# Performance work log

Measured on AMD Instinct MI355X. Metric: run time of the kernel, lower is better.

Reference implementation:

```python
import jax, jax.numpy as jnp
import numpy as np
from jax import lax

RATE = 2
KSIZE = 3
FUSE_K = 3
SOFTMAX_SCALE = 10.0
EPS = 1e-8


def extract_patches(x, k, s):
    """ZeroPad2d(1) then unfold: x [B,C,H,W] -> patches [B, oh*ow, C, k, k]."""
    xp = jnp.pad(x, ((0, 0), (0, 0), (1, 1), (1, 1)))
    B, C, Hp, Wp = xp.shape
    oh = (Hp - k) // s + 1
    ow = (Wp - k) // s + 1
    ii = (jnp.arange(oh) * s)[:, None] + jnp.arange(k)[None, :]   # [oh,k]
    jj = (jnp.arange(ow) * s)[:, None] + jnp.arange(k)[None, :]   # [ow,k]
    p = xp[:, :, ii[:, :, None, None], jj[None, None, :, :]]      # [B,C,oh,k,ow,k]
    p = p.transpose(0, 2, 4, 1, 3, 5).reshape(B, oh * ow, C, k, k)
    return p


def _fuse_conv(a, eye):
    # a: [B,1,N,M]; 3x3 identity-diagonal smoothing conv, padding 1
    return lax.conv_general_dilated(a, eye, (1, 1), [(1, 1), (1, 1)],
                                    dimension_numbers=('NCHW', 'OIHW', 'NCHW'))


def contextual_attention(in_data, mask):
    B, C, H, W = in_data.shape
    Cf = C // 2
    f_full = in_data[:, :Cf]          # narrow(1,0,C//2)
    b_full = in_data[:, :Cf]          # source narrows the SAME slice for b
    mask_f = mask.astype(in_data.dtype)
    rate = RATE
    kernel = 2 * rate

    # raw 4x4 patches of full-res background (deconv filters), [B,L,Cf,4,4]
    raw_w = extract_patches(b_full, kernel, rate)

    # nearest downsample by 1/rate == strided slicing
    f = f_full[:, :, ::rate, ::rate]
    b = b_full[:, :, ::rate, ::rate]
    h, w = f.shape[2], f.shape[3]
    L = h * w

    # 3x3 matching patches of downsampled background, L2-normalized per patch
    wpat = extract_patches(b, KSIZE, 1)                              # [B,L,Cf,3,3]
    norm = jnp.sqrt(jnp.sum(wpat * wpat, axis=(2, 3, 4), keepdims=True))
    wn = wpat / jnp.maximum(norm, EPS)

    # per-sample conv2d(xi, wi_normed, padding=1) == patch/patch correlation
    fp = extract_patches(f, KSIZE, 1)                                # [B,hw,Cf,3,3]
    yi = jnp.einsum('bpckl,bqckl->bqp', fp, wn).reshape(B, L, h, w)  # [B,L,h,w]

    # fuse: two diagonal 3x3 smoothing passes over the [L, h*w] score matrix
    eye = jnp.eye(FUSE_K, dtype=in_data.dtype).reshape(1, 1, FUSE_K, FUSE_K)
    A = yi.reshape(B, 1, L, h * w)
    A = _fuse_conv(A, eye)
    A = A.reshape(B, h, w, h, w).transpose(0, 2, 1, 4, 3).reshape(B, 1, w * h, w * h)
    A = _fuse_conv(A, eye)
    A = A.reshape(B, w, h, w, h).transpose(0, 2, 1, 4, 3)
    yi = A.reshape(B, L, h, w)

    # mask gate: mm = 1 where the 3x3 mask patch is all-zero
    mpat = extract_patches(mask_f, KSIZE, 1)[0]                      # [L,1,3,3]
    m_mean = jnp.mean(mpat, axis=(1, 2, 3))                          # [L]
    mm = (m_mean == 0.0).astype(in_data.dtype)[None, :, None, None]
    yi = yi * mm
    yi = jax.nn.softmax(yi * SOFTMAX_SCALE, axis=1)
    yi = yi * mm

    # conv_transpose2d(yi, raw_wi, stride=rate, padding=1) / 4 per sample
    def agg(y1, rw):
        rhs = jnp.flip(rw, (-2, -1)).transpose(1, 0, 2, 3)           # [Cf,L,4,4]
        return lax.conv_general_dilated(y1[None], rhs, (1, 1), [(2, 2), (2, 2)],
                                        lhs_dilation=(rate, rate),
                                        dimension_numbers=('NCHW', 'OIHW', 'NCHW'))[0]
    y = jax.vmap(agg)(yi, raw_w) / 4.0                               # [B,Cf,H,W]

    # masked_fill_(inv_mask, 0) == multiply by {0,1} mask, upsampled to H x W
    mask_up = jnp.repeat(jnp.repeat(mask_f, rate, axis=2), rate, axis=3)
    y = y * mask_up

    return jnp.concatenate([b_full, f_full, y], axis=1)             # [B,3*Cf,H,W]


def setup_inputs() -> dict:
    key = jax.random.key(0)
    k1, k2 = jax.random.split(key)
    in_data = jax.random.normal(k1, (2, 128, 128, 128), dtype=jnp.float32)
    mask = jax.random.randint(k2, (1, 1, 64, 64), 0, 2, dtype=jnp.int32)
    return {"in_data": in_data, "mask": mask}


def reference(in_data, mask):
    return contextual_attention(in_data, mask)
```

## Files before the change

### kernel.cpp

```cpp
#include <hip/hip_runtime.h>
#include <math.h>

#define MAX_SLOTS 64
#define L 4096

#define OFF_CNT   0
#define OFF_LIST  64
#define OFF_FSUB  512
#define OFF_K5    2230784
#define OFF_SF    3869184
#define OFF_W     5966336

__global__ __launch_bounds__(256) void k_fsub(const float* __restrict__ in,
                                              const int* __restrict__ mask,
                                              int* __restrict__ cnt,
                                              int* __restrict__ list,
                                              float* __restrict__ fsub,
                                              float* __restrict__ sf) {
    int idx = blockIdx.x * 256 + threadIdx.x;
    int j = idx & 63;
    int i = (idx >> 6) & 63;
    int c = (idx >> 12) & 63;
    int b = idx >> 18;
    float v = in[(((b * 128 + c) * 128) + 2 * i) * 128 + 2 * j];
    fsub[(size_t)b * 278784 + c * 4356 + (i + 1) * 66 + (j + 1)] = v;
    sf[idx] = 0.f;
    if (idx < 33280) {
        int plane = idx / 260;
        int r = idx - plane * 260;
        int pb = plane >> 6, pc = plane & 63;
        int row, col;
        if (r < 66) { row = 0; col = r; }
        else if (r < 132) { row = 65; col = r - 66; }
        else { int rr = r - 132; row = (rr >> 1) + 1; col = (rr & 1) ? 65 : 0; }
        fsub[(size_t)pb * 278784 + pc * 4356 + row * 66 + col] = 0.f;
    }
    if (blockIdx.x == 0) {
        __shared__ int lcnt;
        if (threadIdx.x == 0) lcnt = 0;
        __syncthreads();
        for (int q = threadIdx.x; q < L; q += 256) {
            int qi = q >> 6, qj = q & 63;
            bool allz = true;
            for (int dy = -1; dy <= 1; ++dy)
                for (int dx = -1; dx <= 1; ++dx) {
                    int y = qi + dy, x = qj + dx;
                    if (y >= 0 && y < 64 && x >= 0 && x < 64)
                        allz = allz && (mask[y * 64 + x] == 0);
                }
            if (allz) {
                int p = atomicAdd(&lcnt, 1);
                if (p < MAX_SLOTS) list[p] = q;
            }
        }
        __syncthreads();
        if (threadIdx.x == 0) *cnt = (lcnt < MAX_SLOTS) ? lcnt : MAX_SLOTS;
    }
}

__global__ __launch_bounds__(256) void k_prep(const float* __restrict__ fsub,
                                              const int* __restrict__ cnt,
                                              const int* __restrict__ list,
                                              float* __restrict__ K5) {
    int slot = blockIdx.x, b = blockIdx.y;
    int tid = threadIdx.x;
    int nact = min(*cnt, MAX_SLOTS);
    if (slot >= nact) {
        for (int t = tid; t < 1600; t += 256) {
            int c = t / 25, e = t - c * 25;
            K5[(((size_t)b * 64 + c) * 64 + slot) * 25 + e] = 0.f;
        }
        return;
    }
    __shared__ float patch9[9 * 576];
    __shared__ int flag9[9];
    if (tid < 9) flag9[tid] = 0;
    __syncthreads();
    int Q = list[slot];
    const float* F = fsub + (size_t)b * 278784;
    int w = tid >> 6, lane = tid & 63;
    for (int combo = w; combo < 9; combo += 4) {
        int d2 = combo / 3 - 1, d1 = combo % 3 - 1;
        int XQ = ((Q & 63) << 6) + (Q >> 6) + d2;
        if (XQ < 0 || XQ >= L) continue;
        int YQ = ((XQ & 63) << 6) + (XQ >> 6);
        int R = YQ + d1;
        if (R < 0 || R >= L) continue;
        if (lane == 0) flag9[combo] = 1;
        int ri = R >> 6, rj = R & 63;
        const float* Fp = F + ri * 66 + rj;
        float vals[9]; float ss = 0.f;
        #pragma unroll
        for (int k = 0; k < 9; ++k) {
            int t = lane + (k << 6);
            int c = t / 9; int tap = t - c * 9;
            int dy = tap / 3, dx = tap - dy * 3;
            float v = Fp[c * 4356 + dy * 66 + dx];
            vals[k] = v; ss += v * v;
        }
        for (int o = 32; o > 0; o >>= 1) ss += __shfl_xor(ss, o);
        float inv = 1.f / fmaxf(sqrtf(ss), 1e-8f);
        float* dst = patch9 + combo * 576;
        #pragma unroll
        for (int k = 0; k < 9; ++k) dst[lane + (k << 6)] = vals[k] * inv;
    }
    __syncthreads();
    for (int t = tid; t < 1600; t += 256) {
        int c = t / 25, e = t - c * 25;
        int oy = e / 5 - 2, ox = e - (e / 5) * 5 - 2;
        float s = 0.f;
        for (int dy = -1; dy <= 1; ++dy) {
            int dd2 = oy - dy; if (dd2 < -1 || dd2 > 1) continue;
            for (int dx = -1; dx <= 1; ++dx) {
                int dd1 = ox - dx; if (dd1 < -1 || dd1 > 1) continue;
                int combo = (dd2 + 1) * 3 + (dd1 + 1);
                if (flag9[combo])
                    s += patch9[combo * 576 + c * 9 + (dy + 1) * 3 + (dx + 1)];
            }
        }
        K5[(((size_t)b * 64 + c) * 64 + slot) * 25 + e] = s;
    }
}

__global__ __launch_bounds__(64) void k_conv(const float* __restrict__ fsub,
                                             const int* __restrict__ cnt,
                                             const float* __restrict__ K5,
                                             float* __restrict__ sf) {
    int r  = blockIdx.x + 1;
    int cg = blockIdx.y;
    int b  = blockIdx.z;
    int j  = threadIdx.x;
    int nact = min(*cnt, MAX_SLOTS);
    if (nact == 0) return;
    int jc = min(max(j, 1), 62);
    const float* F = fsub + (size_t)b * 278784;
    int base = (r - 1) * 66 + (jc - 1);
    bool active = (j >= 1 && j <= 62);
    int P = (r << 6) + j;
    for (int s0 = 0; s0 < nact; s0 += 16) {
        float acc[16];
        #pragma unroll
        for (int s = 0; s < 16; ++s) acc[s] = 0.f;
        #pragma unroll
        for (int cc = 0; cc < 4; ++cc) {
            int c = cg * 4 + cc;
            const float* Fc = F + c * 4356 + base;
            float win[25];
            #pragma unroll
            for (int dy = 0; dy < 5; ++dy)
                #pragma unroll
                for (int dx = 0; dx < 5; ++dx)
                    win[dy * 5 + dx] = Fc[dy * 66 + dx];
            const float* kc = K5 + (((size_t)b * 64 + c) * 64 + s0) * 25;
            #pragma unroll
            for (int s = 0; s < 16; ++s) {
                #pragma unroll
                for (int k = 0; k < 25; ++k)
                    acc[s] += kc[s * 25 + k] * win[k];
            }
        }
        if (active) {
            int smax = min(16, nact - s0);
            for (int s = 0; s < smax; ++s)
                atomicAdd(&sf[((size_t)b * 64 + (s0 + s)) * 4096 + P], acc[s]);
        }
    }
}

__global__ __launch_bounds__(256) void k_border(const float* __restrict__ fsub,
                                                const int* __restrict__ cnt,
                                                const int* __restrict__ list,
                                                float* __restrict__ sf) {
    int combo = blockIdx.x, slot = blockIdx.y, b = blockIdx.z;
    int tid = threadIdx.x;
    int nact = min(*cnt, MAX_SLOTS);
    if (slot >= nact) return;
    int d2 = combo / 3 - 1, d1 = combo % 3 - 1;
    int Q = list[slot];
    int XQ = ((Q & 63) << 6) + (Q >> 6) + d2;
    if (XQ < 0 || XQ >= L) return;
    int YQ = ((XQ & 63) << 6) + (XQ >> 6);
    int R = YQ + d1;
    if (R < 0 || R >= L) return;
    int ri = R >> 6, rj = R & 63;
    const float* F = fsub + (size_t)b * 278784;
    __shared__ float patch[576];
    __shared__ float red[256];
    __shared__ float s_inv;
    const float* Fp = F + ri * 66 + rj;
    auto ld = [&](int t) -> float {
        int c = t / 9; int tap = t - c * 9;
        int dy = tap / 3, dx = tap - dy * 3;
        return Fp[c * 4356 + dy * 66 + dx];
    };
    float v0 = ld(tid), v1 = ld(tid + 256), v2 = (tid < 64) ? ld(tid + 512) : 0.f;
    red[tid] = v0 * v0 + v1 * v1 + v2 * v2;
    __syncthreads();
    if (tid < 64) {
        float a = red[tid] + red[tid + 64] + red[tid + 128] + red[tid + 192];
        for (int o = 32; o > 0; o >>= 1) a += __shfl_xor(a, o);
        if (tid == 0) s_inv = 1.f / fmaxf(sqrtf(a), 1e-8f);
    }
    __syncthreads();
    float inv = s_inv;
    patch[tid] = v0 * inv; patch[tid + 256] = v1 * inv;
    if (tid < 64) patch[tid + 512] = v2 * inv;
    __syncthreads();
    if (tid >= 252) return;
    int i, j;
    if (tid < 64)       { i = 0;  j = tid; }
    else if (tid < 128) { i = 63; j = tid - 64; }
    else if (tid < 190) { i = tid - 127; j = 0; }
    else                { i = tid - 189; j = 63; }
    int P = (i << 6) + j;
    int XP = (j << 6) + i + d2;
    if (XP < 0 || XP >= L) return;
    int YP = ((XP & 63) << 6) + (XP >> 6);
    int Z = YP + d1;
    if (Z < 0 || Z >= L) return;
    int pi = Z >> 6, pj = Z & 63;
    const float* Fz = F + pi * 66 + pj;
    float dot = 0.f;
    #pragma unroll 4
    for (int c = 0; c < 64; ++c) {
        const float* Fc = Fz + c * 4356;
        const float* pc = patch + c * 9;
        dot += Fc[0] * pc[0]   + Fc[1] * pc[1]   + Fc[2] * pc[2];
        dot += Fc[66] * pc[3]  + Fc[67] * pc[4]  + Fc[68] * pc[5];
        dot += Fc[132] * pc[6] + Fc[133] * pc[7] + Fc[134] * pc[8];
    }
    atomicAdd(&sf[((size_t)b * 64 + slot) * 4096 + P], dot);
}

__global__ __launch_bounds__(256) void k_soft(const int* __restrict__ cnt,
                                              const float* __restrict__ sf,
                                              float* __restrict__ wbuf) {
    int idx = blockIdx.x * 256 + threadIdx.x;
    int b = idx >> 12; int P = idx & 4095;
    int nact = min(*cnt, MAX_SLOTS);
    float M = 0.f;
    for (int s = 0; s < nact; ++s) {
        float l = 10.f * sf[((size_t)b * 64 + s) * 4096 + P];
        M = fmaxf(M, l);
    }
    float denom = (float)(L - nact) * expf(-M);
    for (int s = 0; s < nact; ++s) {
        float e = expf(10.f * sf[((size_t)b * 64 + s) * 4096 + P] - M);
        wbuf[((size_t)b * 64 + s) * 4096 + P] = e;
        denom += e;
    }
    float inv = 1.f / denom;
    for (int s = 0; s < nact; ++s)
        wbuf[((size_t)b * 64 + s) * 4096 + P] *= inv;
}

__global__ __launch_bounds__(128) void k_out(const float* __restrict__ in,
                                             const int* __restrict__ mask,
                                             const int* __restrict__ cnt,
                                             const int* __restrict__ list,
                                             const float* __restrict__ wbuf,
                                             float* __restrict__ out) {
    __shared__ float pat8[MAX_SLOTS * 128];
    int u = blockIdx.x, cg = blockIdx.y, b = blockIdx.z;
    int c0 = cg * 8;
    int tid = threadIdx.x;
    int nact = min(*cnt, MAX_SLOTS);
    const float* inb0 = in + (size_t)b * 2097152 + (size_t)c0 * 16384;
    for (int t = tid; t < nact * 128; t += 128) {
        int s = t >> 7; int r = t & 127;
        int cc = r >> 4; int e = r & 15; int aa = e >> 2; int bb = e & 3;
        int q = list[s]; int qi = q >> 6, qj = q & 63;
        int row = 2 * qi - 1 + aa, col = 2 * qj - 1 + bb;
        float v = (row >= 0 && row < 128 && col >= 0 && col < 128)
                  ? inb0[(size_t)cc * 16384 + row * 128 + col] : 0.f;
        pat8[t] = v;
    }
    __syncthreads();
    int v = tid;
    float y[8];
    #pragma unroll
    for (int cc = 0; cc < 8; ++cc) y[cc] = 0.f;
    if (mask[(u >> 1) * 64 + (v >> 1)] != 0 && nact > 0) {
        int pa = (u + 1) & 1, pb = (v + 1) & 1;
        int i0 = (u + 1 - pa) >> 1, j0 = (v + 1 - pb) >> 1;
        for (int s = 0; s < nact; ++s) {
            const float* wrow = wbuf + ((size_t)b * 64 + s) * 4096;
            const float* ps = pat8 + s * 128;
            #pragma unroll
            for (int di = 0; di < 2; ++di) {
                int i = i0 - di; if (i < 0 || i >= 64) continue;
                int aa = pa + 2 * di;
                #pragma unroll
                for (int dj = 0; dj < 2; ++dj) {
                    int j = j0 - dj; if (j < 0 || j >= 64) continue;
                    float wv = wrow[(i << 6) + j];
                    int tap = aa * 4 + pb + 2 * dj;
                    #pragma unroll
                    for (int cc = 0; cc < 8; ++cc)
                        y[cc] += wv * ps[cc * 16 + tap];
                }
            }
        }
        #pragma unroll
        for (int cc = 0; cc < 8; ++cc) y[cc] *= 0.25f;
    }
    size_t ob = (size_t)(b * 192) * 16384 + (size_t)u * 128 + v;
    #pragma unroll
    for (int cc = 0; cc < 8; ++cc) {
        int c = c0 + cc;
        float val = in[(size_t)(b * 128 + c) * 16384 + u * 128 + v];
        out[ob + (size_t)c * 16384] = val;
        out[ob + (size_t)(c + 64) * 16384] = val;
        out[ob + (size_t)(c + 128) * 16384] = y[cc];
    }
}

extern "C" void kernel_launch(void* const* d_in, const int* in_sizes, int n_in,
                              void* d_out, int out_size, void* d_ws, size_t ws_size,
                              hipStream_t stream) {
    const float* in = (const float*)d_in[0];
    const int* mask = (const int*)d_in[1];
    float* out = (float*)d_out;
    char* ws = (char*)d_ws;
    int* cnt    = (int*)(ws + OFF_CNT);
    int* list   = (int*)(ws + OFF_LIST);
    float* fsub = (float*)(ws + OFF_FSUB);
    float* K5   = (float*)(ws + OFF_K5);
    float* sf   = (float*)(ws + OFF_SF);
    float* wbuf = (float*)(ws + OFF_W);

    k_fsub<<<2048, 256, 0, stream>>>(in, mask, cnt, list, fsub, sf);
    k_prep<<<dim3(MAX_SLOTS, 2), 256, 0, stream>>>(fsub, cnt, list, K5);
    k_conv<<<dim3(62, 16, 2), 64, 0, stream>>>(fsub, cnt, K5, sf);
    k_border<<<dim3(9, MAX_SLOTS, 2), 256, 0, stream>>>(fsub, cnt, list, sf);
    k_soft<<<32, 256, 0, stream>>>(cnt, sf, wbuf);
    k_out<<<dim3(128, 8, 2), 128, 0, stream>>>(in, mask, cnt, list, wbuf, out);
}
```

Baseline: 174.6 us.

## Fuse prep, conv, border, softmax and output into one persistent kernel

Merges the five kernels after initialisation into one persistent kernel with 256 blocks, separated by software grid barriers built on atomic counters. K5 preparation and the border scores now run concurrently on separate block ranges. The softmax is folded into the output stage and recomputed on the fly from the scores, so the weight buffer is no longer written and re-read. This removes launch gaps and a round trip through global memory, but it depends on all 256 blocks being resident at once and recomputes expf three times per element.

```diff
diff --git a/kernel.cpp b/kernel.cpp
--- a/kernel.cpp
+++ b/kernel.cpp
@@ -3,18 +3,20 @@
 
 #define MAX_SLOTS 64
 #define L 4096
+#define NB2 256
 
 #define OFF_CNT   0
 #define OFF_LIST  64
+#define OFF_BAR   384
 #define OFF_FSUB  512
 #define OFF_K5    2230784
 #define OFF_SF    3869184
-#define OFF_W     5966336
-
-__global__ __launch_bounds__(256) void k_fsub(const float* __restrict__ in,
+
+__global__ __launch_bounds__(256) void k_init(const float* __restrict__ in,
                                               const int* __restrict__ mask,
                                               int* __restrict__ cnt,
                                               int* __restrict__ list,
+                                              int* __restrict__ bar,
                                               float* __restrict__ fsub,
                                               float* __restrict__ sf) {
     int idx = blockIdx.x * 256 + threadIdx.x;
@@ -36,6 +38,7 @@
         fsub[(size_t)pb * 278784 + pc * 4356 + row * 66 + col] = 0.f;
     }
     if (blockIdx.x == 0) {
+        if (threadIdx.x < 4) bar[threadIdx.x] = 0;
         __shared__ int lcnt;
         if (threadIdx.x == 0) lcnt = 0;
         __syncthreads();
@@ -58,260 +61,285 @@
     }
 }
 
-__global__ __launch_bounds__(256) void k_prep(const float* __restrict__ fsub,
-                                              const int* __restrict__ cnt,
-                                              const int* __restrict__ list,
-                                              float* __restrict__ K5) {
-    int slot = blockIdx.x, b = blockIdx.y;
+__device__ __forceinline__ void grid_barrier(int* bar, int phase) {
+    __syncthreads();
+    __threadfence();
+    if (threadIdx.x == 0) {
+        __hip_atomic_fetch_add(&bar[phase], 1, __ATOMIC_ACQ_REL, __HIP_MEMORY_SCOPE_AGENT);
+        while (__hip_atomic_load(&bar[phase], __ATOMIC_ACQUIRE, __HIP_MEMORY_SCOPE_AGENT) < NB2)
+            __builtin_amdgcn_s_sleep(2);
+    }
+    __syncthreads();
+    __threadfence();
+}
+
+__global__ __launch_bounds__(256, 2) void k_fused(const float* __restrict__ in,
+                                                  const int* __restrict__ mask,
+                                                  const int* __restrict__ cnt,
+                                                  const int* __restrict__ list,
+                                                  int* __restrict__ bar,
+                                                  const float* __restrict__ fsub,
+                                                  float* __restrict__ K5,
+                                                  float* __restrict__ sf,
+                                                  float* __restrict__ out) {
+    __shared__ float smem[8192];
+    __shared__ int iflags[16];
     int tid = threadIdx.x;
+    int blk = blockIdx.x;
     int nact = min(*cnt, MAX_SLOTS);
-    if (slot >= nact) {
-        for (int t = tid; t < 1600; t += 256) {
-            int c = t / 25, e = t - c * 25;
-            K5[(((size_t)b * 64 + c) * 64 + slot) * 25 + e] = 0.f;
-        }
-        return;
-    }
-    __shared__ float patch9[9 * 576];
-    __shared__ int flag9[9];
-    if (tid < 9) flag9[tid] = 0;
-    __syncthreads();
-    int Q = list[slot];
-    const float* F = fsub + (size_t)b * 278784;
-    int w = tid >> 6, lane = tid & 63;
-    for (int combo = w; combo < 9; combo += 4) {
-        int d2 = combo / 3 - 1, d1 = combo % 3 - 1;
-        int XQ = ((Q & 63) << 6) + (Q >> 6) + d2;
-        if (XQ < 0 || XQ >= L) continue;
-        int YQ = ((XQ & 63) << 6) + (XQ >> 6);
-        int R = YQ + d1;
-        if (R < 0 || R >= L) continue;
-        if (lane == 0) flag9[combo] = 1;
-        int ri = R >> 6, rj = R & 63;
-        const float* Fp = F + ri * 66 + rj;
-        float vals[9]; float ss = 0.f;
+
+    if (blk < 128) {
+        int slot = blk & 63, b = blk >> 6;
+        if (slot >= nact) {
+            for (int t = tid; t < 1600; t += 256) {
+                int c = t / 25, e = t - c * 25;
+                K5[(((size_t)b * 64 + c) * 64 + slot) * 25 + e] = 0.f;
+            }
+        } else {
+            float* patch9 = smem;
+            if (tid < 9) iflags[tid] = 0;
+            __syncthreads();
+            int Q = list[slot];
+            const float* F = fsub + (size_t)b * 278784;
+            int w = tid >> 6, lane = tid & 63;
+            for (int combo = w; combo < 9; combo += 4) {
+                int d2 = combo / 3 - 1, d1 = combo % 3 - 1;
+                int XQ = ((Q & 63) << 6) + (Q >> 6) + d2;
+                if (XQ < 0 || XQ >= L) continue;
+                int YQ = ((XQ & 63) << 6) + (XQ >> 6);
+                int R = YQ + d1;
+                if (R < 0 || R >= L) continue;
+                if (lane == 0) iflags[combo] = 1;
+                int ri = R >> 6, rj = R & 63;
+                const float* Fp = F + ri * 66 + rj;
+                float vals[9]; float ss = 0.f;
+                #pragma unroll
+                for (int k = 0; k < 9; ++k) {
+                    int t = lane + (k << 6);
+                    int c = t / 9; int tap = t - c * 9;
+                    int dy = tap / 3, dx = tap - dy * 3;
+                    float v = Fp[c * 4356 + dy * 66 + dx];
+                    vals[k] = v; ss += v * v;
+                }
+                for (int o = 32; o > 0; o >>= 1) ss += __shfl_xor(ss, o);
+                float inv = 1.f / fmaxf(sqrtf(ss), 1e-8f);
+                float* dst = patch9 + combo * 576;
+                #pragma unroll
+                for (int k = 0; k < 9; ++k) dst[lane + (k << 6)] = vals[k] * inv;
+            }
+            __syncthreads();
+            for (int t = tid; t < 1600; t += 256) {
+                int c = t / 25, e = t - c * 25;
+                int oy = e / 5 - 2, ox = e - (e / 5) * 5 - 2;
+                float s = 0.f;
+                for (int dy = -1; dy <= 1; ++dy) {
+                    int dd2 = oy - dy; if (dd2 < -1 || dd2 > 1) continue;
+                    for (int dx = -1; dx <= 1; ++dx) {
+                        int dd1 = ox - dx; if (dd1 < -1 || dd1 > 1) continue;
+                        int combo = (dd2 + 1) * 3 + (dd1 + 1);
+                        if (iflags[combo])
+                            s += patch9[combo * 576 + c * 9 + (dy + 1) * 3 + (dx + 1)];
+                    }
+                }
+                K5[(((size_t)b * 64 + c) * 64 + slot) * 25 + e] = s;
+            }
+        }
+    } else {
+        for (int bt = blk - 128; bt < 1152; bt += 128) {
+            int combo = bt % 9; int rest = bt / 9;
+            int slot = rest & 63, b = rest >> 6;
+            int d2 = combo / 3 - 1, d1 = combo % 3 - 1;
+            int ri = 0, rj = 0;
+            bool valid = (slot < nact);
+            if (valid) {
+                int Q = list[slot];
+                int XQ = ((Q & 63) << 6) + (Q >> 6) + d2;
+                valid = (XQ >= 0 && XQ < L);
+                if (valid) {
+                    int YQ = ((XQ & 63) << 6) + (XQ >> 6);
+                    int R = YQ + d1;
+                    valid = (R >= 0 && R < L);
+                    if (valid) { ri = R >> 6; rj = R & 63; }
+                }
+            }
+            if (!valid) continue;
+            float* patch = smem;
+            float* red = smem + 576;
+            const float* F = fsub + (size_t)b * 278784;
+            const float* Fp = F + ri * 66 + rj;
+            __syncthreads();
+            auto ld = [&](int t) -> float {
+                int c = t / 9; int tap = t - c * 9;
+                int dy = tap / 3, dx = tap - dy * 3;
+                return Fp[c * 4356 + dy * 66 + dx];
+            };
+            float v0 = ld(tid), v1 = ld(tid + 256), v2 = (tid < 64) ? ld(tid + 512) : 0.f;
+            red[tid] = v0 * v0 + v1 * v1 + v2 * v2;
+            __syncthreads();
+            if (tid < 64) {
+                float a = red[tid] + red[tid + 64] + red[tid + 128] + red[tid + 192];
+                for (int o = 32; o > 0; o >>= 1) a += __shfl_xor(a, o);
+                if (tid == 0) smem[832] = 1.f / fmaxf(sqrtf(a), 1e-8f);
+            }
+            __syncthreads();
+            float inv = smem[832];
+            patch[tid] = v0 * inv; patch[tid + 256] = v1 * inv;
+            if (tid < 64) patch[tid + 512] = v2 * inv;
+            __syncthreads();
+            if (tid < 252) {
+                int i, j;
+                if (tid < 64)       { i = 0;  j = tid; }
+                else if (tid < 128) { i = 63; j = tid - 64; }
+                else if (tid < 190) { i = tid - 127; j = 0; }
+                else                { i = tid - 189; j = 63; }
+                int P = (i << 6) + j;
+                int XP = (j << 6) + i + d2;
+                if (XP >= 0 && XP < L) {
+                    int YP = ((XP & 63) << 6) + (XP >> 6);
+                    int Z = YP + d1;
+                    if (Z >= 0 && Z < L) {
+                        int pi = Z >> 6, pj = Z & 63;
+                        const float* Fz = F + pi * 66 + pj;
+                        float dot = 0.f;
+                        #pragma unroll 4
+                        for (int c = 0; c < 64; ++c) {
+                            const float* Fc = Fz + c * 4356;
+                            const float* pc = patch + c * 9;
+                            dot += Fc[0] * pc[0]   + Fc[1] * pc[1]   + Fc[2] * pc[2];
+                            dot += Fc[66] * pc[3]  + Fc[67] * pc[4]  + Fc[68] * pc[5];
+                            dot += Fc[132] * pc[6] + Fc[133] * pc[7] + Fc[134] * pc[8];
+                        }
+                        atomicAdd(&sf[((size_t)b * 64 + slot) * 4096 + P], dot);
+                    }
+                }
+            }
+        }
+    }
+    grid_barrier(bar, 0);
+
+    {
+        int wid = blk * 4 + (tid >> 6);
+        int j = tid & 63;
+        for (int gw = wid; gw < 1984; gw += NB2 * 4) {
+            int r   = 1 + (gw % 62);
+            int cg2 = (gw / 62) & 15;
+            int b   = gw / 992;
+            int jc = min(max(j, 1), 62);
+            const float* F = fsub + (size_t)b * 278784;
+            int base = (r - 1) * 66 + (jc - 1);
+            bool active = (j >= 1 && j <= 62);
+            int P = (r << 6) + j;
+            for (int s0 = 0; s0 < nact; s0 += 16) {
+                float acc[16];
+                #pragma unroll
+                for (int s = 0; s < 16; ++s) acc[s] = 0.f;
+                #pragma unroll
+                for (int cc = 0; cc < 4; ++cc) {
+                    int c = cg2 * 4 + cc;
+                    const float* Fc = F + c * 4356 + base;
+                    float win[25];
+                    #pragma unroll
+                    for (int dy = 0; dy < 5; ++dy)
+                        #pragma unroll
+                        for (int dx = 0; dx < 5; ++dx)
+                            win[dy * 5 + dx] = Fc[dy * 66 + dx];
+                    const float* kc = K5 + (((size_t)b * 64 + c) * 64 + s0) * 25;
+                    #pragma unroll
+                    for (int s = 0; s < 16; ++s) {
+                        #pragma unroll
+                        for (int k = 0; k < 25; ++k)
+                            acc[s] += kc[s * 25 + k] * win[k];
+                    }
+                }
+                if (active) {
+                    int smax = min(16, nact - s0);
+                    for (int s = 0; s < smax; ++s)
+                        atomicAdd(&sf[((size_t)b * 64 + (s0 + s)) * 4096 + P], acc[s]);
+                }
+            }
+        }
+    }
+    grid_barrier(bar, 1);
+
+    float* pat8 = smem;
+    for (int bt = blk; bt < 1024; bt += NB2) {
+        int up = bt & 63, cg8 = (bt >> 6) & 7, b = bt >> 9;
+        int c0 = cg8 * 8;
+        const float* inb0 = in + (size_t)b * 2097152 + (size_t)c0 * 16384;
+        __syncthreads();
+        for (int t = tid; t < nact * 128; t += 256) {
+            int s = t >> 7; int rr = t & 127;
+            int cc = rr >> 4; int e = rr & 15; int aa = e >> 2; int bb = e & 3;
+            int q = list[s]; int qi = q >> 6, qj = q & 63;
+            int row = 2 * qi - 1 + aa, col = 2 * qj - 1 + bb;
+            float v = (row >= 0 && row < 128 && col >= 0 && col < 128)
+                      ? inb0[(size_t)cc * 16384 + row * 128 + col] : 0.f;
+            pat8[t] = v;
+        }
+        __syncthreads();
+        int uu = tid >> 7, v = tid & 127;
+        int u = up * 2 + uu;
+        float y[8];
         #pragma unroll
-        for (int k = 0; k < 9; ++k) {
-            int t = lane + (k << 6);
-            int c = t / 9; int tap = t - c * 9;
-            int dy = tap / 3, dx = tap - dy * 3;
-            float v = Fp[c * 4356 + dy * 66 + dx];
-            vals[k] = v; ss += v * v;
-        }
-        for (int o = 32; o > 0; o >>= 1) ss += __shfl_xor(ss, o);
-        float inv = 1.f / fmaxf(sqrtf(ss), 1e-8f);
-        float* dst = patch9 + combo * 576;
-        #pragma unroll
-        for (int k = 0; k < 9; ++k) dst[lane + (k << 6)] = vals[k] * inv;
-    }
-    __syncthreads();
-    for (int t = tid; t < 1600; t += 256) {
-        int c = t / 25, e = t - c * 25;
-        int oy = e / 5 - 2, ox = e - (e / 5) * 5 - 2;
-        float s = 0.f;
-        for (int dy = -1; dy <= 1; ++dy) {
-            int dd2 = oy - dy; if (dd2 < -1 || dd2 > 1) continue;
-            for (int dx = -1; dx <= 1; ++dx) {
-                int dd1 = ox - dx; if (dd1 < -1 || dd1 > 1) continue;
-                int combo = (dd2 + 1) * 3 + (dd1 + 1);
-                if (flag9[combo])
-                    s += patch9[combo * 576 + c * 9 + (dy + 1) * 3 + (dx + 1)];
-            }
-        }
-        K5[(((size_t)b * 64 + c) * 64 + slot) * 25 + e] = s;
-    }
-}
-
-__global__ __launch_bounds__(64) void k_conv(const float* __restrict__ fsub,
-                                             const int* __restrict__ cnt,
-                                             const float* __restrict__ K5,
-                                             float* __restrict__ sf) {
-    int r  = blockIdx.x + 1;
-    int cg = blockIdx.y;
-    int b  = blockIdx.z;
-    int j  = threadIdx.x;
-    int nact = min(*cnt, MAX_SLOTS);
-    if (nact == 0) return;
-    int jc = min(max(j, 1), 62);
-    const float* F = fsub + (size_t)b * 278784;
-    int base = (r - 1) * 66 + (jc - 1);
-    bool active = (j >= 1 && j <= 62);
-    int P = (r << 6) + j;
-    for (int s0 = 0; s0 < nact; s0 += 16) {
-        float acc[16];
-        #pragma unroll
-        for (int s = 0; s < 16; ++s) acc[s] = 0.f;
-        #pragma unroll
-        for (int cc = 0; cc < 4; ++cc) {
-            int c = cg * 4 + cc;
-            const float* Fc = F + c * 4356 + base;
-            float win[25];
+        for (int cc = 0; cc < 8; ++cc) y[cc] = 0.f;
+        if (mask[(u >> 1) * 64 + (v >> 1)] != 0 && nact > 0) {
+            int pa = (u + 1) & 1, pb = (v + 1) & 1;
+            int i0 = (u + 1 - pa) >> 1, j0 = (v + 1 - pb) >> 1;
+            int Pp[4]; int tap[4]; bool val[4];
             #pragma unroll
-            for (int dy = 0; dy < 5; ++dy)
-                #pragma unroll
-                for (int dx = 0; dx < 5; ++dx)
-                    win[dy * 5 + dx] = Fc[dy * 66 + dx];
-            const float* kc = K5 + (((size_t)b * 64 + c) * 64 + s0) * 25;
+            for (int di = 0; di < 2; ++di)
+                #pragma unroll
+                for (int dj = 0; dj < 2; ++dj) {
+                    int p = di * 2 + dj;
+                    int i = i0 - di, j = j0 - dj;
+                    val[p] = (i >= 0 && i < 64 && j >= 0 && j < 64);
+                    Pp[p] = val[p] ? ((i << 6) + j) : 0;
+                    tap[p] = (pa + 2 * di) * 4 + (pb + 2 * dj);
+                }
+            const float* sfb = sf + (size_t)b * 64 * 4096;
+            float Mx[4] = {0.f, 0.f, 0.f, 0.f};
+            for (int s = 0; s < nact; ++s) {
+                const float* srow = sfb + (size_t)s * 4096;
+                #pragma unroll
+                for (int p = 0; p < 4; ++p)
+                    if (val[p]) Mx[p] = fmaxf(Mx[p], 10.f * srow[Pp[p]]);
+            }
+            float den[4];
             #pragma unroll
-            for (int s = 0; s < 16; ++s) {
-                #pragma unroll
-                for (int k = 0; k < 25; ++k)
-                    acc[s] += kc[s * 25 + k] * win[k];
-            }
-        }
-        if (active) {
-            int smax = min(16, nact - s0);
-            for (int s = 0; s < smax; ++s)
-                atomicAdd(&sf[((size_t)b * 64 + (s0 + s)) * 4096 + P], acc[s]);
-        }
-    }
-}
-
-__global__ __launch_bounds__(256) void k_border(const float* __restrict__ fsub,
-                                                const int* __restrict__ cnt,
-                                                const int* __restrict__ list,
-                                                float* __restrict__ sf) {
-    int combo = blockIdx.x, slot = blockIdx.y, b = blockIdx.z;
-    int tid = threadIdx.x;
-    int nact = min(*cnt, MAX_SLOTS);
-    if (slot >= nact) return;
-    int d2 = combo / 3 - 1, d1 = combo % 3 - 1;
-    int Q = list[slot];
-    int XQ = ((Q & 63) << 6) + (Q >> 6) + d2;
-    if (XQ < 0 || XQ >= L) return;
-    int YQ = ((XQ & 63) << 6) + (XQ >> 6);
-    int R = YQ + d1;
-    if (R < 0 || R >= L) return;
-    int ri = R >> 6, rj = R & 63;
-    const float* F = fsub + (size_t)b * 278784;
-    __shared__ float patch[576];
-    __shared__ float red[256];
-    __shared__ float s_inv;
-    const float* Fp = F + ri * 66 + rj;
-    auto ld = [&](int t) -> float {
-        int c = t / 9; int tap = t - c * 9;
-        int dy = tap / 3, dx = tap - dy * 3;
-        return Fp[c * 4356 + dy * 66 + dx];
-    };
-    float v0 = ld(tid), v1 = ld(tid + 256), v2 = (tid < 64) ? ld(tid + 512) : 0.f;
-    red[tid] = v0 * v0 + v1 * v1 + v2 * v2;
-    __syncthreads();
-    if (tid < 64) {
-        float a = red[tid] + red[tid + 64] + red[tid + 128] + red[tid + 192];
-        for (int o = 32; o > 0; o >>= 1) a += __shfl_xor(a, o);
-        if (tid == 0) s_inv = 1.f / fmaxf(sqrtf(a), 1e-8f);
-    }
-    __syncthreads();
-    float inv = s_inv;
-    patch[tid] = v0 * inv; patch[tid + 256] = v1 * inv;
-    if (tid < 64) patch[tid + 512] = v2 * inv;
-    __syncthreads();
-    if (tid >= 252) return;
-    int i, j;
-    if (tid < 64)       { i = 0;  j = tid; }
-    else if (tid < 128) { i = 63; j = tid - 64; }
-    else if (tid < 190) { i = tid - 127; j = 0; }
-    else                { i = tid - 189; j = 63; }
-    int P = (i << 6) + j;
-    int XP = (j << 6) + i + d2;
-    if (XP < 0 || XP >= L) return;
-    int YP = ((XP & 63) << 6) + (XP >> 6);
-    int Z = YP + d1;
-    if (Z < 0 || Z >= L) return;
-    int pi = Z >> 6, pj = Z & 63;
-    const float* Fz = F + pi * 66 + pj;
-    float dot = 0.f;
-    #pragma unroll 4
-    for (int c = 0; c < 64; ++c) {
-        const float* Fc = Fz + c * 4356;
-        const float* pc = patch + c * 9;
-        dot += Fc[0] * pc[0]   + Fc[1] * pc[1]   + Fc[2] * pc[2];
-        dot += Fc[66] * pc[3]  + Fc[67] * pc[4]  + Fc[68] * pc[5];
-        dot += Fc[132] * pc[6] + Fc[133] * pc[7] + Fc[134] * pc[8];
-    }
-    atomicAdd(&sf[((size_t)b * 64 + slot) * 4096 + P], dot);
-}
-
-__global__ __launch_bounds__(256) void k_soft(const int* __restrict__ cnt,
-                                              const float* __restrict__ sf,
-                                              float* __restrict__ wbuf) {
-    int idx = blockIdx.x * 256 + threadIdx.x;
-    int b = idx >> 12; int P = idx & 4095;
-    int nact = min(*cnt, MAX_SLOTS);
-    float M = 0.f;
-    for (int s = 0; s < nact; ++s) {
-        float l = 10.f * sf[((size_t)b * 64 + s) * 4096 + P];
-        M = fmaxf(M, l);
-    }
-    float denom = (float)(L - nact) * expf(-M);
-    for (int s = 0; s < nact; ++s) {
-        float e = expf(10.f * sf[((size_t)b * 64 + s) * 4096 + P] - M);
-        wbuf[((size_t)b * 64 + s) * 4096 + P] = e;
-        denom += e;
-    }
-    float inv = 1.f / denom;
-    for (int s = 0; s < nact; ++s)
-        wbuf[((size_t)b * 64 + s) * 4096 + P] *= inv;
-}
-
-__global__ __launch_bounds__(128) void k_out(const float* __restrict__ in,
-                                             const int* __restrict__ mask,
-                                             const int* __restrict__ cnt,
-                                             const int* __restrict__ list,
-                                             const float* __restrict__ wbuf,
-                                             float* __restrict__ out) {
-    __shared__ float pat8[MAX_SLOTS * 128];
-    int u = blockIdx.x, cg = blockIdx.y, b = blockIdx.z;
-    int c0 = cg * 8;
-    int tid = threadIdx.x;
-    int nact = min(*cnt, MAX_SLOTS);
-    const float* inb0 = in + (size_t)b * 2097152 + (size_t)c0 * 16384;
-    for (int t = tid; t < nact * 128; t += 128) {
-        int s = t >> 7; int r = t & 127;
-        int cc = r >> 4; int e = r & 15; int aa = e >> 2; int bb = e & 3;
-        int q = list[s]; int qi = q >> 6, qj = q & 63;
-        int row = 2 * qi - 1 + aa, col = 2 * qj - 1 + bb;
-        float v = (row >= 0 && row < 128 && col >= 0 && col < 128)
-                  ? inb0[(size_t)cc * 16384 + row * 128 + col] : 0.f;
-        pat8[t] = v;
-    }
-    __syncthreads();
-    int v = tid;
-    float y[8];
-    #pragma unroll
-    for (int cc = 0; cc < 8; ++cc) y[cc] = 0.f;
-    if (mask[(u >> 1) * 64 + (v >> 1)] != 0 && nact > 0) {
-        int pa = (u + 1) & 1, pb = (v + 1) & 1;
-        int i0 = (u + 1 - pa) >> 1, j0 = (v + 1 - pb) >> 1;
-        for (int s = 0; s < nact; ++s) {
-            const float* wrow = wbuf + ((size_t)b * 64 + s) * 4096;
-            const float* ps = pat8 + s * 128;
+            for (int p = 0; p < 4; ++p) den[p] = (float)(L - nact) * expf(-Mx[p]);
+            for (int s = 0; s < nact; ++s) {
+                const float* srow = sfb + (size_t)s * 4096;
+                #pragma unroll
+                for (int p = 0; p < 4; ++p)
+                    if (val[p]) den[p] += expf(10.f * srow[Pp[p]] - Mx[p]);
+            }
+            float inv[4];
             #pragma unroll
-            for (int di = 0; di < 2; ++di) {
-                int i = i0 - di; if (i < 0 || i >= 64) continue;
-                int aa = pa + 2 * di;
-                #pragma unroll
-                for (int dj = 0; dj < 2; ++dj) {
-                    int j = j0 - dj; if (j < 0 || j >= 64) continue;
-                    float wv = wrow[(i << 6) + j];
-                    int tap = aa * 4 + pb + 2 * dj;
+            for (int p = 0; p < 4; ++p) inv[p] = val[p] ? 1.f / den[p] : 0.f;
+            for (int s = 0; s < nact; ++s) {
+                const float* srow = sfb + (size_t)s * 4096;
+                const float* ps = pat8 + s * 128;
+                #pragma unroll
+                for (int p = 0; p < 4; ++p) {
+                    if (!val[p]) continue;
+                    float wv = expf(10.f * srow[Pp[p]] - Mx[p]) * inv[p];
                     #pragma unroll
                     for (int cc = 0; cc < 8; ++cc)
-                        y[cc] += wv * ps[cc * 16 + tap];
-                }
-            }
-        }
+                        y[cc] += wv * ps[cc * 16 + tap[p]];
+                }
+            }
+            #pragma unroll
+            for (int cc = 0; cc < 8; ++cc) y[cc] *= 0.25f;
+        }
+        size_t ob = (size_t)(b * 192) * 16384 + (size_t)u * 128 + v;
         #pragma unroll
-        for (int cc = 0; cc < 8; ++cc) y[cc] *= 0.25f;
-    }
-    size_t ob = (size_t)(b * 192) * 16384 + (size_t)u * 128 + v;
-    #pragma unroll
-    for (int cc = 0; cc < 8; ++cc) {
-        int c = c0 + cc;
-        float val = in[(size_t)(b * 128 + c) * 16384 + u * 128 + v];
-        out[ob + (size_t)c * 16384] = val;
-        out[ob + (size_t)(c + 64) * 16384] = val;
-        out[ob + (size_t)(c + 128) * 16384] = y[cc];
+        for (int cc = 0; cc < 8; ++cc) {
+            int c = c0 + cc;
+            float pval = in[(size_t)(b * 128 + c) * 16384 + u * 128 + v];
+            out[ob + (size_t)c * 16384] = pval;
+            out[ob + (size_t)(c + 64) * 16384] = pval;
+            out[ob + (size_t)(c + 128) * 16384] = y[cc];
+        }
     }
 }
 
@@ -324,15 +352,11 @@
     char* ws = (char*)d_ws;
     int* cnt    = (int*)(ws + OFF_CNT);
     int* list   = (int*)(ws + OFF_LIST);
+    int* bar    = (int*)(ws + OFF_BAR);
     float* fsub = (float*)(ws + OFF_FSUB);
     float* K5   = (float*)(ws + OFF_K5);
     float* sf   = (float*)(ws + OFF_SF);
-    float* wbuf = (float*)(ws + OFF_W);
-
-    k_fsub<<<2048, 256, 0, stream>>>(in, mask, cnt, list, fsub, sf);
-    k_prep<<<dim3(MAX_SLOTS, 2), 256, 0, stream>>>(fsub, cnt, list, K5);
-    k_conv<<<dim3(62, 16, 2), 64, 0, stream>>>(fsub, cnt, K5, sf);
-    k_border<<<dim3(9, MAX_SLOTS, 2), 256, 0, stream>>>(fsub, cnt, list, sf);
-    k_soft<<<32, 256, 0, stream>>>(cnt, sf, wbuf);
-    k_out<<<dim3(128, 8, 2), 128, 0, stream>>>(in, mask, cnt, list, wbuf, out);
+
+    k_init<<<2048, 256, 0, stream>>>(in, mask, cnt, list, bar, fsub, sf);
+    k_fused<<<NB2, 256, 0, stream>>>(in, mask, cnt, list, bar, fsub, K5, sf, out);
 }
```

Result: slower. 576.3 us (+230.1%).
